# Kernel tuning notes

Measured on AMD Instinct MI355X. Metric: run time of the kernel, lower is better.

The kernel has to match this reference:

```python
import jax, jax.numpy as jnp
import numpy as np

NEG = -1e9
BN_EPS = 1e-5


def conv1d(x, w, b):
    # x: [B, C, L], w: [O, I, K], b: [O]; 'same' padding (K//2)
    k = w.shape[-1]
    y = jax.lax.conv_general_dilated(
        x, w, window_strides=(1,), padding=[(k // 2, k // 2)],
        dimension_numbers=("NCH", "OIH", "NCH"))
    return y + b[None, :, None]


def sparsemax(z):
    # sparsemax along last axis (Martins & Astudillo 2016)
    z = z - jnp.max(z, axis=-1, keepdims=True)  # shift-invariant, for stability
    zs = jnp.flip(jnp.sort(z, axis=-1), axis=-1)  # descending
    cs = jnp.cumsum(zs, axis=-1)
    L = z.shape[-1]
    rng = jnp.arange(1, L + 1, dtype=z.dtype)
    support = (1.0 + rng * zs) > cs
    k_z = jnp.sum(support, axis=-1, keepdims=True)  # int support size, >=1
    cs_k = jnp.take_along_axis(cs, k_z - 1, axis=-1)
    tau = (cs_k - 1.0) / k_z.astype(z.dtype)
    return jnp.maximum(z - tau, 0.0)


def setup_inputs() -> dict:
    key = jax.random.key(0)
    ks = jax.random.split(key, 12)
    B, D, L, H, OUT, K = 32, 1024, 1024, 32, 11, 7
    s_conv = 1.0 / np.sqrt(D * K)
    s_lin = 1.0 / np.sqrt(2 * D)
    s_out = 1.0 / np.sqrt(H)
    return {
        "x": jax.random.normal(ks[0], (B, D, L), jnp.float32),
        "mask": jax.random.randint(ks[1], (B, L), 0, 2) > 0,
        "conv1_w": jax.random.normal(ks[2], (D, D, K), jnp.float32) * s_conv,
        "conv1_b": jax.random.normal(ks[3], (D,), jnp.float32) * s_conv,
        "attend_w": jax.random.normal(ks[4], (D, D, K), jnp.float32) * s_conv,
        "attend_b": jax.random.normal(ks[5], (D,), jnp.float32) * s_conv,
        "lin_w": jax.random.normal(ks[6], (H, 2 * D), jnp.float32) * s_lin,
        "lin_b": jax.random.normal(ks[7], (H,), jnp.float32) * s_lin,
        "bn_gamma": jnp.ones((H,), jnp.float32),
        "bn_beta": jnp.zeros((H,), jnp.float32),
        "bn_mean": jnp.zeros((H,), jnp.float32),
        "bn_var": jnp.ones((H,), jnp.float32),
        "out_w": jax.random.normal(ks[8], (OUT, H), jnp.float32) * s_out,
        "out_b": jax.random.normal(ks[9], (OUT,), jnp.float32) * s_out,
    }


def reference(x, mask, conv1_w, conv1_b, attend_w, attend_b, lin_w, lin_b,
              bn_gamma, bn_beta, bn_mean, bn_var, out_w, out_b):
    # dropout layers are identity at inference
    o = conv1d(x, conv1_w, conv1_b)                       # [B, D, L]
    att = conv1d(x, attend_w, attend_b)                   # [B, D, L]
    att = jnp.where(mask[:, None, :], att, NEG)
    p = sparsemax(att)                                    # [B, D, L]
    o1 = jnp.sum(o * p, axis=-1)                          # [B, D]
    o2 = jnp.max(o, axis=-1)                              # [B, D]
    h = jnp.concatenate([o1, o2], axis=-1)                # [B, 2D]
    h = h @ lin_w.T + lin_b                               # [B, 32]
    h = jax.nn.relu(h)
    h = (h - bn_mean) * jax.lax.rsqrt(bn_var + BN_EPS) * bn_gamma + bn_beta
    return h @ out_w.T + out_b                            # [B, 11]
```

## Files before the change

kernel.cpp:

```cpp
#include <hip/hip_runtime.h>
#include <hip/hip_bf16.h>
#include <stdint.h>

typedef _Float16 f16x8 __attribute__((ext_vector_type(8)));
typedef float f32x4 __attribute__((ext_vector_type(4)));

#define AS1 __attribute__((address_space(1)))
#define AS3 __attribute__((address_space(3)))

__device__ __forceinline__ void glds16(const void* g, void* l) {
  __builtin_amdgcn_global_load_lds((const AS1 unsigned int*)g,
                                   (AS3 unsigned int*)l, 16, 0, 0);
}

#define NEGV -1e9f

__global__ void k_wt(const float* __restrict__ w1, const float* __restrict__ w2,
                     _Float16* __restrict__ Wt) {
  int c = blockIdx.x >> 10;
  int dout = blockIdx.x & 1023;
  const float* w = (c == 0) ? w1 : w2;
  for (int t = 0; t < 4; ++t) {
    int din = threadIdx.x + t * 256;
    const float* s = w + ((size_t)dout * 1024 + din) * 7;
#pragma unroll
    for (int k = 0; k < 7; ++k)
      Wt[(((size_t)(c * 7 + k)) << 20) + (size_t)dout * 1024 + din] = (_Float16)s[k];
  }
}

__global__ void k_zero_halo(_Float16* __restrict__ xT) {
  _Float16* p = xT + (size_t)blockIdx.x * (1032 * 1024);
  for (int i = threadIdx.x; i < 8192; i += 256) {
    int r = i >> 10;
    int cidx = i & 1023;
    int row = (r < 4) ? r : (1024 + r);
    p[(size_t)row * 1024 + cidx] = (_Float16)0.f;
  }
}

__global__ void k_transpose(const float* __restrict__ x, _Float16* __restrict__ xT, int b0) {
  __shared__ float t[64][65];
  int bl = blockIdx.z;
  int l0 = blockIdx.x * 64, d0 = blockIdx.y * 64;
  const float* xb = x + (size_t)(b0 + bl) * 1024 * 1024;
  int c4 = (threadIdx.x & 15) * 4;
  int r0 = threadIdx.x >> 4;
#pragma unroll
  for (int s = 0; s < 4; ++s) {
    int row = r0 + s * 16;
    float4 v = *(const float4*)(xb + (size_t)(d0 + row) * 1024 + l0 + c4);
    t[row][c4 + 0] = v.x; t[row][c4 + 1] = v.y; t[row][c4 + 2] = v.z; t[row][c4 + 3] = v.w;
  }
  __syncthreads();
  _Float16* xo = xT + (size_t)bl * (1032 * 1024);
#pragma unroll
  for (int s = 0; s < 4; ++s) {
    int lrow = r0 + s * 16;
    union { ushort4 u; _Float16 h[4]; } pk;
    pk.h[0] = (_Float16)t[c4 + 0][lrow];
    pk.h[1] = (_Float16)t[c4 + 1][lrow];
    pk.h[2] = (_Float16)t[c4 + 2][lrow];
    pk.h[3] = (_Float16)t[c4 + 3][lrow];
    *(ushort4*)(xo + (size_t)(l0 + lrow + 4) * 1024 + d0 + c4) = pk.u;
  }
}

__launch_bounds__(256, 2)
__global__ void k_conv(const _Float16* __restrict__ xT, const _Float16* __restrict__ Wt,
                       float* __restrict__ obuf, float* __restrict__ abuf) {
  __shared__ _Float16 xs[2][136 * 64];
  __shared__ _Float16 wsm[2][128 * 64];
  int tid = threadIdx.x;
  int n0 = blockIdx.x * 128;
  int m0 = blockIdx.y * 128;
  int bz = blockIdx.z;
  int bl = bz >> 1, c = bz & 1;
  const _Float16* xb = xT + (size_t)bl * (1032 * 1024);
  const _Float16* wb = Wt + ((size_t)(c * 7) << 20);

  auto stageW = [&](int k, int cc, int buf) {
    const _Float16* src = wb + ((size_t)k << 20) + (size_t)m0 * 1024 + cc * 64;
    _Float16* dst = &wsm[buf][0];
#pragma unroll
    for (int ii = 0; ii < 4; ++ii) {
      int idx = ii * 256 + tid;
      int r = idx >> 3, cb = (idx & 7) << 3;
      glds16(src + (size_t)r * 1024 + (cb ^ ((r & 7) << 3)), dst + (size_t)idx * 8);
    }
  };
  auto stageX = [&](int cc, int buf) {
    const _Float16* src = xb + (size_t)n0 * 1024 + cc * 64;
    _Float16* dst = &xs[buf][0];
#pragma unroll
    for (int ii = 0; ii < 5; ++ii) {
      int idx = ii * 256 + tid;
      if (idx < 1088) {
        int r = idx >> 3, cb = (idx & 7) << 3;
        glds16(src + (size_t)r * 1024 + (cb ^ ((r & 7) << 3)), dst + (size_t)idx * 8);
      }
    }
  };

  f32x4 acc[4][4];
#pragma unroll
  for (int i = 0; i < 4; ++i)
#pragma unroll
    for (int j = 0; j < 4; ++j) acc[i][j] = (f32x4){0.f, 0.f, 0.f, 0.f};

  int lane = tid & 63, wid = tid >> 6;
  int wr = wid >> 1, wc = wid & 1;
  int col = lane & 15, kq = lane >> 4;
  int arow0 = wr * 64 + col;
  int swA = (col & 7) << 3;
  int brow0 = wc * 64 + col + 1;

  stageX(0, 0);
  stageW(0, 0, 0);
  __syncthreads();

  for (int it = 0; it < 112; ++it) {
    int cc = it / 7, k = it - cc * 7;
    if (it + 1 < 112) {
      int itn = it + 1;
      int ccn = itn / 7, kn = itn - ccn * 7;
      stageW(kn, ccn, itn & 1);
      if (ccn != cc) stageX(ccn, ccn & 1);
    }
    const _Float16* wp = &wsm[it & 1][0];
    const _Float16* xp = &xs[cc & 1][0];
    int brow = brow0 + k;
#pragma unroll
    for (int g = 0; g < 2; ++g) {
      int eo = g * 32 + kq * 8;
      f16x8 A[4], Bv[4];
#pragma unroll
      for (int i = 0; i < 4; ++i) {
        int r = arow0 + i * 16;
        A[i] = *(const f16x8*)(wp + (size_t)r * 64 + (eo ^ swA));
      }
#pragma unroll
      for (int j = 0; j < 4; ++j) {
        int r = brow + j * 16;
        Bv[j] = *(const f16x8*)(xp + (size_t)r * 64 + (eo ^ ((r & 7) << 3)));
      }
#pragma unroll
      for (int i = 0; i < 4; ++i)
#pragma unroll
        for (int j = 0; j < 4; ++j)
          acc[i][j] = __builtin_amdgcn_mfma_f32_16x16x32_f16(A[i], Bv[j], acc[i][j], 0, 0, 0);
    }
    __syncthreads();
  }

  float* ob = (c == 0 ? obuf : abuf) + (size_t)bl * 1024 * 1024;
  int dr0 = m0 + wr * 64 + kq * 4;
  int l0o = n0 + wc * 64 + col;
#pragma unroll
  for (int i = 0; i < 4; ++i)
#pragma unroll
    for (int j = 0; j < 4; ++j)
#pragma unroll
      for (int r = 0; r < 4; ++r)
        ob[(size_t)(dr0 + i * 16 + r) * 1024 + l0o + j * 16] = acc[i][j][r];
}

__global__ void k_rows(const float* __restrict__ obuf, const float* __restrict__ abuf,
                       const void* __restrict__ maskp, const float* __restrict__ conv_b,
                       float* __restrict__ hbuf, int b0) {
  int wid = threadIdx.x >> 6, lane = threadIdx.x & 63;
  int row = blockIdx.x * 4 + wid;
  int bl = row >> 10, d = row & 1023;
  int bg = b0 + bl;

  unsigned wdet = ((const unsigned*)maskp)[lane];
  int isBool = __any((int)((wdet & 0xFFFFFF00u) != 0));

  const float* ar = abuf + (size_t)row * 1024;
  float z[16];
#pragma unroll
  for (int t = 0; t < 4; ++t) {
    float4 v = *(const float4*)(ar + t * 256 + lane * 4);
    z[t * 4 + 0] = v.x; z[t * 4 + 1] = v.y; z[t * 4 + 2] = v.z; z[t * 4 + 3] = v.w;
  }
  if (isBool) {
    const unsigned char* mb = (const unsigned char*)maskp + (size_t)bg * 1024;
#pragma unroll
    for (int t = 0; t < 4; ++t) {
      unsigned m4 = *(const unsigned*)(mb + t * 256 + lane * 4);
      if (!(m4 & 0x000000FFu)) z[t * 4 + 0] = NEGV;
      if (!(m4 & 0x0000FF00u)) z[t * 4 + 1] = NEGV;
      if (!(m4 & 0x00FF0000u)) z[t * 4 + 2] = NEGV;
      if (!(m4 & 0xFF000000u)) z[t * 4 + 3] = NEGV;
    }
  } else {
    const int* mi = (const int*)maskp + (size_t)bg * 1024;
#pragma unroll
    for (int t = 0; t < 4; ++t) {
      int4 m = *(const int4*)(mi + t * 256 + lane * 4);
      if (!m.x) z[t * 4 + 0] = NEGV;
      if (!m.y) z[t * 4 + 1] = NEGV;
      if (!m.z) z[t * 4 + 2] = NEGV;
      if (!m.w) z[t * 4 + 3] = NEGV;
    }
  }

  float zmax = z[0];
#pragma unroll
  for (int q = 1; q < 16; ++q) zmax = fmaxf(zmax, z[q]);
  for (int o = 32; o; o >>= 1) zmax = fmaxf(zmax, __shfl_xor(zmax, o));

  float lo = zmax - 1.0f, hi = zmax;
  for (int itn = 0; itn < 26; ++itn) {
    float mid = 0.5f * (lo + hi);
    float f = 0.f;
#pragma unroll
    for (int q = 0; q < 16; ++q) f += fmaxf(z[q] - mid, 0.f);
    for (int o = 32; o; o >>= 1) f += __shfl_xor(f, o);
    if (f >= 1.0f) lo = mid; else hi = mid;
  }
  float s = 0.f, kc = 0.f;
#pragma unroll
  for (int q = 0; q < 16; ++q)
    if (z[q] > lo) { s += z[q]; kc += 1.f; }
  for (int o = 32; o; o >>= 1) { s += __shfl_xor(s, o); kc += __shfl_xor(kc, o); }
  float tau = (s - 1.0f) / kc;

  const float* orow = obuf + (size_t)row * 1024;
  float o1 = 0.f, o2 = -1e30f;
#pragma unroll
  for (int t = 0; t < 4; ++t) {
    float4 v = *(const float4*)(orow + t * 256 + lane * 4);
    o1 += v.x * fmaxf(z[t * 4 + 0] - tau, 0.f); o2 = fmaxf(o2, v.x);
    o1 += v.y * fmaxf(z[t * 4 + 1] - tau, 0.f); o2 = fmaxf(o2, v.y);
    o1 += v.z * fmaxf(z[t * 4 + 2] - tau, 0.f); o2 = fmaxf(o2, v.z);
    o1 += v.w * fmaxf(z[t * 4 + 3] - tau, 0.f); o2 = fmaxf(o2, v.w);
  }
  for (int o = 32; o; o >>= 1) {
    o1 += __shfl_xor(o1, o);
    o2 = fmaxf(o2, __shfl_xor(o2, o));
  }
  if (lane == 0) {
    float bb = conv_b[d];
    hbuf[(size_t)bg * 2048 + d] = o1 + bb;
    hbuf[(size_t)bg * 2048 + 1024 + d] = o2 + bb;
  }
}

__global__ void k_final(const float* __restrict__ hbuf, const float* __restrict__ lw,
                        const float* __restrict__ lb, const float* __restrict__ bg,
                        const float* __restrict__ bb, const float* __restrict__ bm,
                        const float* __restrict__ bv, const float* __restrict__ ow,
                        const float* __restrict__ obv, float* __restrict__ out) {
  int b = blockIdx.x, lane = threadIdx.x;
  const float* hb = hbuf + (size_t)b * 2048;
  __shared__ float yy[32];
  for (int j = 0; j < 32; ++j) {
    float p = 0.f;
    for (int t = 0; t < 32; ++t) p += hb[t * 64 + lane] * lw[(size_t)j * 2048 + t * 64 + lane];
    for (int o = 32; o; o >>= 1) p += __shfl_xor(p, o);
    if (lane == 0) yy[j] = p + lb[j];
  }
  __syncthreads();
  float v = 0.f;
  if (lane < 32) {
    v = fmaxf(yy[lane], 0.f);
    v = (v - bm[lane]) * rsqrtf(bv[lane] + 1e-5f) * bg[lane] + bb[lane];
  }
  for (int o = 0; o < 11; ++o) {
    float t = (lane < 32) ? v * ow[o * 32 + lane] : 0.f;
    for (int off = 32; off; off >>= 1) t += __shfl_xor(t, off);
    if (lane == 0) out[b * 11 + o] = t + obv[o];
  }
}

static inline int imin(int a, int b) { return a < b ? a : b; }

extern "C" void kernel_launch(void* const* d_in, const int* in_sizes, int n_in,
                              void* d_out, int out_size, void* d_ws, size_t ws_size,
                              hipStream_t stream) {
  const float* x = (const float*)d_in[0];
  const void* mask = d_in[1];
  const float* w1 = (const float*)d_in[2];
  const float* b1 = (const float*)d_in[3];
  const float* w2 = (const float*)d_in[4];
  const float* lin_w = (const float*)d_in[6];
  const float* lin_b = (const float*)d_in[7];
  const float* bn_g = (const float*)d_in[8];
  const float* bn_b = (const float*)d_in[9];
  const float* bn_m = (const float*)d_in[10];
  const float* bn_v = (const float*)d_in[11];
  const float* out_w = (const float*)d_in[12];
  const float* out_b = (const float*)d_in[13];
  float* out = (float*)d_out;

  char* ws = (char*)d_ws;
  _Float16* Wt = (_Float16*)ws;
  size_t off = (size_t)2 * 7 * 1024 * 1024 * 2;
  float* hbuf = (float*)(ws + off);
  off += (size_t)32 * 2048 * 4;
  size_t fixed = off;
  size_t per_b = (size_t)1032 * 1024 * 2 + (size_t)2 * 1024 * 1024 * 4;

  long avail = (long)ws_size - (long)fixed;
  int bc = (avail > 0) ? (int)(avail / (long)per_b) : 1;
  if (bc < 1) bc = 1;
  if (bc > 32) bc = 32;

  _Float16* xT = (_Float16*)(ws + fixed);
  float* obuf = (float*)(ws + fixed + (size_t)bc * 1032 * 1024 * 2);
  float* abuf = obuf + (size_t)bc * 1024 * 1024;

  k_wt<<<2048, 256, 0, stream>>>(w1, w2, Wt);

  for (int b0 = 0; b0 < 32; b0 += bc) {
    int nb = imin(bc, 32 - b0);
    k_zero_halo<<<nb, 256, 0, stream>>>(xT);
    k_transpose<<<dim3(16, 16, nb), 256, 0, stream>>>(x, xT, b0);
    k_conv<<<dim3(8, 8, nb * 2), 256, 0, stream>>>(xT, Wt, obuf, abuf);
    k_rows<<<nb * 256, 256, 0, stream>>>(obuf, abuf, mask, b1, hbuf, b0);
  }
  k_final<<<32, 64, 0, stream>>>(hbuf, lin_w, lin_b, bn_g, bn_b, bn_m, bn_v, out_w, out_b, out);
}
```

Measured before the change: 1.373 ms.

## Enlarge conv GEMM tile to 256x256 with phased prefetch and MFMA priority

The conv GEMM kernel moves from a 128x128 tile with 256 threads to a 256x256 tile with 512 threads. Each wave now holds a 128x64 accumulator block. The x operand is reloaded per kernel tap (shifted rows) instead of staged once per channel chunk and indexed with an offset. The next stage's global-to-LDS loads are interleaved across four compute phases with explicit vmcnt waits, barriers and s_setprio around the MFMA bursts. The aim is more operand reuse per byte loaded and better overlap of loads with MFMA work. The risks are higher register pressure (128 accumulator floats per thread), only 4x4 blocks per batch on the grid, and x being re-read seven times per chunk.

```diff
diff --git a/kernel.cpp b/kernel.cpp
--- a/kernel.cpp
+++ b/kernel.cpp
@@ -66,103 +66,124 @@
   }
 }
 
-__launch_bounds__(256, 2)
+__launch_bounds__(512, 2)
 __global__ void k_conv(const _Float16* __restrict__ xT, const _Float16* __restrict__ Wt,
                        float* __restrict__ obuf, float* __restrict__ abuf) {
-  __shared__ _Float16 xs[2][136 * 64];
-  __shared__ _Float16 wsm[2][128 * 64];
+  __shared__ _Float16 smem[2][2][16384];
   int tid = threadIdx.x;
-  int n0 = blockIdx.x * 128;
-  int m0 = blockIdx.y * 128;
+  int n0 = blockIdx.x * 256;
+  int m0 = blockIdx.y * 256;
   int bz = blockIdx.z;
   int bl = bz >> 1, c = bz & 1;
   const _Float16* xb = xT + (size_t)bl * (1032 * 1024);
   const _Float16* wb = Wt + ((size_t)(c * 7) << 20);
 
-  auto stageW = [&](int k, int cc, int buf) {
-    const _Float16* src = wb + ((size_t)k << 20) + (size_t)m0 * 1024 + cc * 64;
-    _Float16* dst = &wsm[buf][0];
-#pragma unroll
-    for (int ii = 0; ii < 4; ++ii) {
-      int idx = ii * 256 + tid;
-      int r = idx >> 3, cb = (idx & 7) << 3;
-      glds16(src + (size_t)r * 1024 + (cb ^ ((r & 7) << 3)), dst + (size_t)idx * 8);
+  int lane = tid & 63, wid = tid >> 6;
+  int wr = wid >> 2;
+  int wcol = wid & 3;
+  int col = lane & 15, kq = lane >> 4;
+  int swA = (col & 7) << 3;
+
+  auto stg = [&](const _Float16* src, _Float16* dst, int li) {
+    int e = li * 512 + tid;
+    int r = e >> 3, cb = (e & 7) << 3;
+    glds16(src + (size_t)r * 1024 + (cb ^ ((r & 7) << 3)), dst + (size_t)e * 8);
+  };
+
+  f32x4 acc[8][4];
+#pragma unroll
+  for (int i = 0; i < 8; ++i)
+#pragma unroll
+    for (int j = 0; j < 4; ++j) acc[i][j] = (f32x4){0.f, 0.f, 0.f, 0.f};
+
+  {
+    const _Float16* pA = wb + (size_t)m0 * 1024;
+    const _Float16* pB = xb + (size_t)(n0 + 1) * 1024;
+    stg(pB, &smem[0][1][0], 0); stg(pB, &smem[0][1][0], 1);
+    stg(pB, &smem[0][1][0], 2); stg(pB, &smem[0][1][0], 3);
+    stg(pA, &smem[0][0][0], 0); stg(pA, &smem[0][0][0], 2);
+    stg(pA, &smem[0][0][0], 1); stg(pA, &smem[0][0][0], 3);
+  }
+  asm volatile("s_waitcnt vmcnt(2)" ::: "memory");
+  __builtin_amdgcn_s_barrier();
+
+#define CPHASE(MB, S1, S2, TAIL)                                              \
+  {                                                                           \
+    f16x8 Af[2][2];                                                           \
+    _Pragma("unroll") for (int i = 0; i < 2; ++i)                             \
+    _Pragma("unroll") for (int g = 0; g < 2; ++g) {                           \
+      int R = wr * 128 + (MB + i) * 16 + col;                                 \
+      Af[i][g] = *(const f16x8*)(Ab + (size_t)R * 64 +                        \
+                                 (((g << 5) + (kq << 3)) ^ swA));             \
+    }                                                                         \
+    S1; S2;                                                                   \
+    __builtin_amdgcn_s_barrier();                                             \
+    __builtin_amdgcn_s_setprio(1);                                            \
+    _Pragma("unroll") for (int g = 0; g < 2; ++g)                             \
+    _Pragma("unroll") for (int i = 0; i < 2; ++i)                             \
+    _Pragma("unroll") for (int j = 0; j < 4; ++j)                             \
+      acc[MB + i][j] = __builtin_amdgcn_mfma_f32_16x16x32_f16(                \
+          Af[i][g], Bf[j][g], acc[MB + i][j], 0, 0, 0);                       \
+    __builtin_amdgcn_s_setprio(0);                                            \
+    TAIL;                                                                     \
+    __builtin_amdgcn_s_barrier();                                             \
+  }
+
+  for (int t = 0; t < 112; ++t) {
+    int cur = t & 1;
+    const _Float16* Ab = &smem[cur][0][0];
+    const _Float16* Bb = &smem[cur][1][0];
+    _Float16* nAd = &smem[cur ^ 1][0][0];
+    _Float16* nBd = &smem[cur ^ 1][1][0];
+    const _Float16* nA = nullptr;
+    const _Float16* nB = nullptr;
+    bool hasNext = (t + 1 < 112);
+    if (hasNext) {
+      int s2 = t + 1, cc2 = s2 / 7, k2 = s2 - cc2 * 7;
+      nA = wb + ((size_t)k2 << 20) + (size_t)m0 * 1024 + (size_t)cc2 * 64;
+      nB = xb + (size_t)(n0 + k2 + 1) * 1024 + (size_t)cc2 * 64;
     }
-  };
-  auto stageX = [&](int cc, int buf) {
-    const _Float16* src = xb + (size_t)n0 * 1024 + cc * 64;
-    _Float16* dst = &xs[buf][0];
-#pragma unroll
-    for (int ii = 0; ii < 5; ++ii) {
-      int idx = ii * 256 + tid;
-      if (idx < 1088) {
-        int r = idx >> 3, cb = (idx & 7) << 3;
-        glds16(src + (size_t)r * 1024 + (cb ^ ((r & 7) << 3)), dst + (size_t)idx * 8);
+
+    f16x8 Bf[4][2];
+#pragma unroll
+    for (int j = 0; j < 4; ++j)
+#pragma unroll
+      for (int g = 0; g < 2; ++g) {
+        int R = wcol * 64 + j * 16 + col;
+        Bf[j][g] = *(const f16x8*)(Bb + (size_t)R * 64 +
+                                   (((g << 5) + (kq << 3)) ^ swA));
       }
-    }
-  };
-
-  f32x4 acc[4][4];
-#pragma unroll
-  for (int i = 0; i < 4; ++i)
-#pragma unroll
-    for (int j = 0; j < 4; ++j) acc[i][j] = (f32x4){0.f, 0.f, 0.f, 0.f};
-
-  int lane = tid & 63, wid = tid >> 6;
-  int wr = wid >> 1, wc = wid & 1;
-  int col = lane & 15, kq = lane >> 4;
-  int arow0 = wr * 64 + col;
-  int swA = (col & 7) << 3;
-  int brow0 = wc * 64 + col + 1;
-
-  stageX(0, 0);
-  stageW(0, 0, 0);
-  __syncthreads();
-
-  for (int it = 0; it < 112; ++it) {
-    int cc = it / 7, k = it - cc * 7;
-    if (it + 1 < 112) {
-      int itn = it + 1;
-      int ccn = itn / 7, kn = itn - ccn * 7;
-      stageW(kn, ccn, itn & 1);
-      if (ccn != cc) stageX(ccn, ccn & 1);
-    }
-    const _Float16* wp = &wsm[it & 1][0];
-    const _Float16* xp = &xs[cc & 1][0];
-    int brow = brow0 + k;
-#pragma unroll
-    for (int g = 0; g < 2; ++g) {
-      int eo = g * 32 + kq * 8;
-      f16x8 A[4], Bv[4];
-#pragma unroll
-      for (int i = 0; i < 4; ++i) {
-        int r = arow0 + i * 16;
-        A[i] = *(const f16x8*)(wp + (size_t)r * 64 + (eo ^ swA));
-      }
-#pragma unroll
-      for (int j = 0; j < 4; ++j) {
-        int r = brow + j * 16;
-        Bv[j] = *(const f16x8*)(xp + (size_t)r * 64 + (eo ^ ((r & 7) << 3)));
-      }
-#pragma unroll
-      for (int i = 0; i < 4; ++i)
-#pragma unroll
-        for (int j = 0; j < 4; ++j)
-          acc[i][j] = __builtin_amdgcn_mfma_f32_16x16x32_f16(A[i], Bv[j], acc[i][j], 0, 0, 0);
-    }
-    __syncthreads();
-  }
+
+    CPHASE(0,
+           if (hasNext) stg(nB, nBd, 0),
+           if (hasNext) stg(nB, nBd, 1),
+           );
+    CPHASE(2,
+           if (hasNext) stg(nB, nBd, 2),
+           if (hasNext) stg(nB, nBd, 3),
+           if (hasNext) { asm volatile("s_waitcnt vmcnt(4)" ::: "memory"); }
+           else        { asm volatile("s_waitcnt vmcnt(0)" ::: "memory"); });
+    CPHASE(4,
+           if (hasNext) stg(nA, nAd, 0),
+           if (hasNext) stg(nA, nAd, 2),
+           );
+    CPHASE(6,
+           if (hasNext) stg(nA, nAd, 1),
+           if (hasNext) stg(nA, nAd, 3),
+           if (hasNext) { asm volatile("s_waitcnt vmcnt(2)" ::: "memory"); });
+  }
+#undef CPHASE
 
   float* ob = (c == 0 ? obuf : abuf) + (size_t)bl * 1024 * 1024;
-  int dr0 = m0 + wr * 64 + kq * 4;
-  int l0o = n0 + wc * 64 + col;
-#pragma unroll
-  for (int i = 0; i < 4; ++i)
+  int r0 = m0 + wr * 128 + kq * 4;
+  int c0 = n0 + wcol * 64 + col;
+#pragma unroll
+  for (int m = 0; m < 8; ++m)
 #pragma unroll
     for (int j = 0; j < 4; ++j)
 #pragma unroll
       for (int r = 0; r < 4; ++r)
-        ob[(size_t)(dr0 + i * 16 + r) * 1024 + l0o + j * 16] = acc[i][j][r];
+        ob[(size_t)(r0 + m * 16 + r) * 1024 + c0 + j * 16] = acc[m][j][r];
 }
 
 __global__ void k_rows(const float* __restrict__ obuf, const float* __restrict__ abuf,
@@ -317,7 +338,7 @@
     int nb = imin(bc, 32 - b0);
     k_zero_halo<<<nb, 256, 0, stream>>>(xT);
     k_transpose<<<dim3(16, 16, nb), 256, 0, stream>>>(x, xT, b0);
-    k_conv<<<dim3(8, 8, nb * 2), 256, 0, stream>>>(xT, Wt, obuf, abuf);
+    k_conv<<<dim3(4, 4, nb * 2), 512, 0, stream>>>(xT, Wt, obuf, abuf);
     k_rows<<<nb * 256, 256, 0, stream>>>(obuf, abuf, mask, b1, hbuf, b0);
   }
   k_final<<<32, 64, 0, stream>>>(hbuf, lin_w, lin_b, bn_g, bn_b, bn_m, bn_v, out_w, out_b, out);
```

Result: faster. 1.148 ms (-16.4%).
